# Optimization experiments

Measured on AMD Instinct MI355X. Metric: run time of the kernel, lower is better.

Reference implementation:

```python
import jax, jax.numpy as jnp
import numpy as np

N, EG, T, H, EC, L, NT = 10000, 200000, 300000, 128, 128, 3, 100


def _ssp(x):
    # ShiftedSoftplus: softplus(x) - log(2)
    return jax.nn.softplus(x) - jnp.log(2.0).astype(x.dtype)


def _bn(x, g, b):
    # BatchNorm1d in training mode: biased batch stats, eps=1e-5
    m = jnp.mean(x, axis=0)
    v = jnp.var(x, axis=0)
    return g * (x - m) * jax.lax.rsqrt(v + 1e-5) + b


def _forward(z, i, j, idx_i, idx_j, idx_k, idx_ji, idx_kj, pos,
             We1, be1, We2, be2, We3, be3,
             Wc1, bc1, g_c1, b_c1, g_n, b_n,
             Wc2, bc2, g_c2, b_c2, Wc3, bc3, g_c3, b_c3,
             g_c22, b_c22, g_c32, b_c32,
             Wf1, bf1, Wf2, bf2, Wf3, bf3):
    # AtomType2NodeEmb
    h = jax.nn.one_hot(z, NT, dtype=jnp.float32)
    h = _ssp(h @ We1 + be1)
    h = _ssp(h @ We2 + be2)
    node = h @ We3 + be3                      # [N, H]
    # geometry + GaussianFilter edge embedding
    rel = pos[i] - pos[j]                     # [EG, 3]
    dist = jnp.sqrt(jnp.sum(rel * rel, axis=-1))
    unit = rel / dist[:, None]
    offset = jnp.linspace(0.0, 5.0, EC)
    coeff = -0.5 / (offset[1] - offset[0]) ** 2
    edge = jnp.exp(coeff * (dist[:, None] - offset[None, :]) ** 2)  # [EG, EC]
    for l in range(L):
        # NodeUpdate
        c1 = jnp.concatenate([node[i], edge], axis=1) @ Wc1[l] + bc1[l]
        c1 = _bn(c1, g_c1[l], b_c1[l])
        f1, r1 = jnp.split(c1, 2, axis=1)
        agg = jax.ops.segment_sum(jax.nn.sigmoid(f1) * jnp.tanh(r1), i, num_segments=N)
        node = jnp.tanh(node + _bn(agg, g_n[l], b_n[l]))
        # EdgeUpdate: pair term
        c2 = (node[i] * node[j]) @ Wc2[l] + bc2[l]
        c2 = _bn(c2, g_c2[l], b_c2[l])
        f2, r2 = jnp.split(c2, 2, axis=1)
        c2_emb = _bn(jax.nn.sigmoid(f2) * jnp.tanh(r2), g_c22[l], b_c22[l])
        # EdgeUpdate: triplet term
        c3 = jnp.concatenate([node[idx_i], node[idx_j], node[idx_k],
                              edge[idx_ji], edge[idx_kj]], axis=1) @ Wc3[l] + bc3[l]
        c3 = _bn(c3, g_c3[l], b_c3[l])
        f3, r3 = jnp.split(c3, 2, axis=1)
        agg3 = jax.ops.segment_sum(jax.nn.sigmoid(f3) * jnp.tanh(r3), idx_ji, num_segments=EG)
        c3_emb = _bn(agg3, g_c32[l], b_c32[l])
        edge = jnp.tanh(edge + c2_emb + c3_emb)
    # ForcePredictor
    f = _ssp(edge @ Wf1 + bf1)
    f = _ssp(f @ Wf2 + bf2)
    force = (f @ Wf3 + bf3) * unit            # [EG, 3]
    return jax.ops.segment_sum(force, i, num_segments=N)


def setup_inputs() -> dict:
    ks = iter(jax.random.split(jax.random.key(0), 32))

    def w(shape):
        return jax.random.normal(next(ks), shape, jnp.float32) * (shape[-2] ** -0.5)

    z = jax.random.randint(next(ks), (N,), 0, NT)
    pos = jax.random.uniform(next(ks), (N, 3), jnp.float32) * 5.0
    i = jax.random.randint(next(ks), (EG,), 0, N)
    j = (i + 1 + jax.random.randint(next(ks), (EG,), 0, N - 1)) % N  # no self-loops
    idx_i = jax.random.randint(next(ks), (T,), 0, N)
    idx_j = jax.random.randint(next(ks), (T,), 0, N)
    idx_k = jax.random.randint(next(ks), (T,), 0, N)
    idx_ji = jax.random.randint(next(ks), (T,), 0, EG)
    idx_kj = jax.random.randint(next(ks), (T,), 0, EG)
    return dict(
        z=z, pos=pos, i=i, j=j, idx_i=idx_i, idx_j=idx_j, idx_k=idx_k,
        idx_ji=idx_ji, idx_kj=idx_kj,
        We1=w((NT, H)), be1=jnp.zeros((H,)), We2=w((H, H)), be2=jnp.zeros((H,)),
        We3=w((H, H)), be3=jnp.zeros((H,)),
        Wc1=w((L, H + EC, 2 * H)), bc1=jnp.zeros((L, 2 * H)),
        g_c1=jnp.ones((L, 2 * H)), b_c1=jnp.zeros((L, 2 * H)),
        g_n=jnp.ones((L, H)), b_n=jnp.zeros((L, H)),
        Wc2=w((L, H, 2 * EC)), bc2=jnp.zeros((L, 2 * EC)),
        g_c2=jnp.ones((L, 2 * EC)), b_c2=jnp.zeros((L, 2 * EC)),
        Wc3=w((L, 3 * H + 2 * EC, 2 * EC)), bc3=jnp.zeros((L, 2 * EC)),
        g_c3=jnp.ones((L, 2 * EC)), b_c3=jnp.zeros((L, 2 * EC)),
        g_c22=jnp.ones((L, EC)), b_c22=jnp.zeros((L, EC)),
        g_c32=jnp.ones((L, EC)), b_c32=jnp.zeros((L, EC)),
        Wf1=w((EC, EC)), bf1=jnp.zeros((EC,)), Wf2=w((EC, EC)), bf2=jnp.zeros((EC,)),
        Wf3=w((EC, 1)), bf3=jnp.zeros((1,)),
    )


def reference(z, pos, i, j, idx_i, idx_j, idx_k, idx_ji, idx_kj,
              We1, be1, We2, be2, We3, be3,
              Wc1, bc1, g_c1, b_c1, g_n, b_n,
              Wc2, bc2, g_c2, b_c2, Wc3, bc3, g_c3, b_c3,
              g_c22, b_c22, g_c32, b_c32,
              Wf1, bf1, Wf2, bf2, Wf3, bf3):
    return _forward(z, i, j, idx_i, idx_j, idx_k, idx_ji, idx_kj, pos,
                    We1, be1, We2, be2, We3, be3,
                    Wc1, bc1, g_c1, b_c1, g_n, b_n,
                    Wc2, bc2, g_c2, b_c2, Wc3, bc3, g_c3, b_c3,
                    g_c22, b_c22, g_c32, b_c32,
                    Wf1, bf1, Wf2, bf2, Wf3, bf3)
```

## Files before the change

kernel.cpp:

```cpp
#include <hip/hip_runtime.h>

typedef unsigned short u16;
typedef unsigned int   u32;
typedef __attribute__((ext_vector_type(8))) short short8;
typedef __attribute__((ext_vector_type(4))) float f32x4;

#define NN  10000
#define EGN 200000
#define TTN 300000
#define LLN 3

__device__ __forceinline__ float b2f(u16 u){ union{u32 i; float f;} x; x.i=(u32)u<<16; return x.f; }
__device__ __forceinline__ u16 f2b(float f){ union{float f; u32 u;} x; x.f=f; u32 r=(x.u + 0x7fffu + ((x.u>>16)&1u))>>16; return (u16)r; }
__device__ __forceinline__ float sigf(float x){ return 1.f/(1.f+__expf(-x)); }
__device__ __forceinline__ float tanhf_(float x){ float e=__expf(2.f*x); return 1.f - 2.f/(e+1.f); }
__device__ __forceinline__ float sspf(float x){ return fmaxf(x,0.f) + log1pf(__expf(-fabsf(x))) - 0.6931471805599453f; }

__device__ __forceinline__ void async16(void* lds, const void* g){
  __builtin_amdgcn_global_load_lds((const __attribute__((address_space(1))) void*)g,
                                   (__attribute__((address_space(3))) void*)lds, 16, 0, 0);
}
__device__ __forceinline__ void split_store(float v, u16* ph, u16* pl, size_t o){
  u16 h = f2b(v); ph[o] = h; pl[o] = f2b(v - b2f(h));
}
__device__ __forceinline__ short8 ldfrag(const u16* P, int row, int kk, int lane){
  int kg = kk*4 + (lane>>4);
  int slot = kg ^ (row&7);
  return *(const short8*)(P + row*64 + slot*8);
}

struct Segs {
  const u16* sh[10];
  const u16* sl[10];
  const int* idx[10];
  int coff[10];
};

template<int NP, int ROWS>
__device__ __forceinline__ void stageA(u16* Ah, u16* Al,
    const u16* sh, const u16* sl, const int* idxp, int coff,
    int rb, int M, int tid){
#pragma unroll
  for (int rnd=0; rnd<ROWS/32; ++rnd){
    int u = rnd*256 + tid;
    int row = u>>3, s = u&7, sw = s ^ (row&7);
    int grow = rb + row; if (grow >= M) grow = M-1;
    int srow = idxp ? idxp[grow] : grow;
    size_t go = (size_t)srow*256 + coff + sw*16;
    async16(Ah + u*8, (const char*)sh + go);
    if (NP==2) async16(Al + u*8, (const char*)sl + go);
  }
}

template<int NP, int ROWS>
__device__ __forceinline__ void stageA_prod(u16* Ah, u16* Al,
    const u16* nh, const u16* nl, const int* pii, const int* pjj,
    int rb, int M, int ks, int tid){
#pragma unroll
  for (int rep=0; rep<ROWS/64; ++rep){
    int row = rep*64 + (tid>>2), q = tid&3;
    int e = rb + row; if (e >= M) e = M-1;
    int ia = pii[e], ja = pjj[e];
    const u16* phi = nh + (size_t)ia*128 + ks*64 + q*16;
    const u16* pli = nl + (size_t)ia*128 + ks*64 + q*16;
    const u16* phj = nh + (size_t)ja*128 + ks*64 + q*16;
    const u16* plj = nl + (size_t)ja*128 + ks*64 + q*16;
#pragma unroll
    for (int c=0;c<2;c++){
      short8 hi = *(const short8*)(phi + c*8);
      short8 li = *(const short8*)(pli + c*8);
      short8 hj = *(const short8*)(phj + c*8);
      short8 lj = *(const short8*)(plj + c*8);
      short8 vh, vl;
#pragma unroll
      for (int k=0;k<8;k++){
        float a = b2f((u16)hi[k]) + b2f((u16)li[k]);
        float b = b2f((u16)hj[k]) + b2f((u16)lj[k]);
        float v = a*b;
        u16 h = f2b(v);
        vh[k] = (short)h;
        vl[k] = (short)f2b(v - b2f(h));
      }
      int g = q*2 + c, slot = g ^ (row&7);
      *(short8*)(Ah + row*64 + slot*8) = vh;
      if (NP==2) *(short8*)(Al + row*64 + slot*8) = vl;
    }
  }
}

template<int NP, int BROWS>
__device__ __forceinline__ void stageB_id(u16* Bh, u16* Bl,
    const u16* Wh, const u16* Wl, int K2b, int ksoff, int tid){
#pragma unroll
  for (int rnd=0; rnd<BROWS/32; ++rnd){
    int u = rnd*256 + tid;
    int row = u>>3, s = u&7, sw = s ^ (row&7);
    size_t go = (size_t)row*K2b + ksoff + sw*16;
    async16(Bh + u*8, (const char*)Wh + go);
    if (NP==2) async16(Bl + u*8, (const char*)Wl + go);
  }
}

template<int NP>
__device__ __forceinline__ void stageB_pair(u16* Bh, u16* Bl,
    const u16* Wh, const u16* Wl, int P0, int K2b, int ksoff, int tid){
#pragma unroll
  for (int rnd=0; rnd<4; ++rnd){
    int u = rnd*256 + tid;
    int row = u>>3, s = u&7, sw = s ^ (row&7);
    int wr = (row < 64) ? (P0 + row) : (128 + P0 + (row-64));
    size_t go = (size_t)wr*K2b + ksoff + sw*16;
    async16(Bh + u*8, (const char*)Wh + go);
    if (NP==2) async16(Bl + u*8, (const char*)Wl + go);
  }
}

template<bool PROD>
__global__ __launch_bounds__(256) void gemm_stats(
  int M, int nseg, Segs segs,
  const u16* __restrict__ nh, const u16* __restrict__ nl,
  const int* __restrict__ pii, const int* __restrict__ pjj,
  const u16* __restrict__ Wh, int K2b, const float* __restrict__ bias,
  float* __restrict__ st)
{
  __shared__ u16 Ah[64*64];
  __shared__ u16 Bh[256*64];
  __shared__ float ls[256], lq[256];
  const int tid = threadIdx.x, lane = tid&63, wv = tid>>6;
  const int rb = blockIdx.x*64;
  ls[tid]=0.f; lq[tid]=0.f;

  f32x4 acc[16];
#pragma unroll
  for (int n=0;n<16;n++) acc[n] = (f32x4){0.f,0.f,0.f,0.f};

  for (int ks=0; ks<nseg; ++ks){
    if (PROD) stageA_prod<1,64>(Ah, nullptr, nh, nl, pii, pjj, rb, M, ks, tid);
    else      stageA<1,64>(Ah, nullptr, segs.sh[ks], nullptr, segs.idx[ks], segs.coff[ks], rb, M, tid);
    stageB_id<1,256>(Bh, nullptr, Wh, nullptr, K2b, ks*128, tid);
    __syncthreads();
    const int arow = wv*16 + (lane&15);
#pragma unroll
    for (int kk=0;kk<2;kk++){
      short8 a = ldfrag(Ah, arow, kk, lane);
#pragma unroll
      for (int n=0;n<16;n++){
        short8 b = ldfrag(Bh, n*16 + (lane&15), kk, lane);
        acc[n] = __builtin_amdgcn_mfma_f32_16x16x32_bf16(a, b, acc[n], 0,0,0);
      }
    }
    __syncthreads();
  }
#pragma unroll
  for (int n=0;n<16;n++){
    float bb = bias[n*16 + (lane&15)];
    float s=0.f, q=0.f;
#pragma unroll
    for (int r=0;r<4;r++){
      int grow = rb + wv*16 + (lane>>4)*4 + r;
      if (grow < M){ float v = acc[n][r] + bb; s += v; q += v*v; }
    }
    s += __shfl_xor(s,16); s += __shfl_xor(s,32);
    q += __shfl_xor(q,16); q += __shfl_xor(q,32);
    if (lane < 16){ atomicAdd(&ls[n*16+lane], s); atomicAdd(&lq[n*16+lane], q); }
  }
  __syncthreads();
  atomicAdd(&st[tid], ls[tid]); atomicAdd(&st[256+tid], lq[tid]);
}

template<int NP, bool PROD, int EPI>
__global__ __launch_bounds__(256) void gemm_pair(
  int M, int nseg, Segs segs,
  const u16* __restrict__ nh, const u16* __restrict__ nl,
  const int* __restrict__ pii, const int* __restrict__ pjj,
  const u16* __restrict__ Wh, const u16* __restrict__ Wl, int K2b,
  const float* __restrict__ bias,
  const float* __restrict__ st, const float* __restrict__ g, const float* __restrict__ b, float inv,
  const int* __restrict__ sidx, float* __restrict__ aggout,
  const float* __restrict__ st22, const float* __restrict__ g22, const float* __restrict__ b22,
  const float* __restrict__ st32, const float* __restrict__ g32, const float* __restrict__ b32, float inv2,
  const float* __restrict__ agg3, u16* __restrict__ eh, u16* __restrict__ el,
  float* __restrict__ st22out)
{
  __shared__ u16 Ah[128*64];
  __shared__ u16 Al[NP==2 ? 128*64 : 64];
  __shared__ u16 Bh[128*64];
  __shared__ u16 Bl[NP==2 ? 128*64 : 64];
  __shared__ float ls[64], lq[64];
  __shared__ float sAf[64], sCf[64], sAr[64], sCr[64];
  __shared__ float sA22[64], sC22[64], sA32[64], sC32[64];
  const int tid = threadIdx.x, lane = tid&63, wv = tid>>6;
  const int wm = wv>>1, wn = wv&1;
  const int rb = blockIdx.x*128, P0 = blockIdx.y*64;

  if (tid < 64){
    int p = P0 + tid;
    float m1 = st[p]*inv,     v1 = st[256+p]*inv - m1*m1;
    float a1 = g[p]*rsqrtf(v1+1e-5f);
    sAf[tid]=a1; sCf[tid]=b[p]-a1*m1;
    float m2 = st[128+p]*inv, v2 = st[384+p]*inv - m2*m2;
    float a2 = g[128+p]*rsqrtf(v2+1e-5f);
    sAr[tid]=a2; sCr[tid]=b[128+p]-a2*m2;
    if (EPI==1){
      float m3 = st22[p]*inv2, v3 = st22[128+p]*inv2 - m3*m3;
      float a3 = g22[p]*rsqrtf(v3+1e-5f);
      sA22[tid]=a3; sC22[tid]=b22[p]-a3*m3;
      float m4 = st32[p]*inv2, v4 = st32[128+p]*inv2 - m4*m4;
      float a4 = g32[p]*rsqrtf(v4+1e-5f);
      sA32[tid]=a4; sC32[tid]=b32[p]-a4*m4;
    }
    if (EPI==2){ ls[tid]=0.f; lq[tid]=0.f; }
  }

  f32x4 accf[4][2], accr[4][2];
#pragma unroll
  for (int m=0;m<4;m++)
#pragma unroll
    for (int n=0;n<2;n++){ accf[m][n]=(f32x4){0.f,0.f,0.f,0.f}; accr[m][n]=(f32x4){0.f,0.f,0.f,0.f}; }

  for (int ks=0; ks<nseg; ++ks){
    if (PROD) stageA_prod<NP,128>(Ah, Al, nh, nl, pii, pjj, rb, M, ks, tid);
    else      stageA<NP,128>(Ah, Al, segs.sh[ks], segs.sl[ks], segs.idx[ks], segs.coff[ks], rb, M, tid);
    stageB_pair<NP>(Bh, Bl, Wh, Wl, P0, K2b, ks*128, tid);
    __syncthreads();
#pragma unroll
    for (int kk=0;kk<2;kk++){
      short8 ah[4], al[4];
#pragma unroll
      for (int m=0;m<4;m++){
        int ar = wm*64 + m*16 + (lane&15);
        ah[m] = ldfrag(Ah, ar, kk, lane);
        if constexpr (NP==2) al[m] = ldfrag(Al, ar, kk, lane);
      }
#pragma unroll
      for (int n=0;n<2;n++){
        int brf = wn*32 + n*16 + (lane&15);
        short8 bfh = ldfrag(Bh, brf,    kk, lane);
        short8 brh = ldfrag(Bh, 64+brf, kk, lane);
        short8 bfl, brl;
        if constexpr (NP==2){ bfl = ldfrag(Bl, brf, kk, lane); brl = ldfrag(Bl, 64+brf, kk, lane); }
#pragma unroll
        for (int m=0;m<4;m++){
          accf[m][n] = __builtin_amdgcn_mfma_f32_16x16x32_bf16(ah[m], bfh, accf[m][n], 0,0,0);
          accr[m][n] = __builtin_amdgcn_mfma_f32_16x16x32_bf16(ah[m], brh, accr[m][n], 0,0,0);
          if constexpr (NP==2){
            accf[m][n] = __builtin_amdgcn_mfma_f32_16x16x32_bf16(ah[m], bfl, accf[m][n], 0,0,0);
            accf[m][n] = __builtin_amdgcn_mfma_f32_16x16x32_bf16(al[m], bfh, accf[m][n], 0,0,0);
            accr[m][n] = __builtin_amdgcn_mfma_f32_16x16x32_bf16(ah[m], brl, accr[m][n], 0,0,0);
            accr[m][n] = __builtin_amdgcn_mfma_f32_16x16x32_bf16(al[m], brh, accr[m][n], 0,0,0);
          }
        }
      }
    }
    __syncthreads();
  }

#pragma unroll
  for (int n=0;n<2;n++){
    const int pp = wn*32 + n*16 + (lane&15);
    const int p  = P0 + pp;
    const float bf_ = bias[p], br_ = bias[128+p];
    const float Af = sAf[pp], Cf = sCf[pp], Ar = sAr[pp], Cr = sCr[pp];
    float su=0.f, sq=0.f;
#pragma unroll
    for (int m=0;m<4;m++){
#pragma unroll
      for (int r=0;r<4;r++){
        int grow = rb + wm*64 + m*16 + (lane>>4)*4 + r;
        if (grow < M){
          float yf = accf[m][n][r] + bf_;
          float yr = accr[m][n][r] + br_;
          float u = sigf(Af*yf + Cf) * tanhf_(Ar*yr + Cr);
          if (EPI==0){
            atomicAdd(&aggout[(size_t)sidx[grow]*128 + p], u);
          } else if (EPI==1){
            size_t o = (size_t)grow*128 + p;
            float eo = b2f(eh[o]) + b2f(el[o]);
            float v = tanhf_(eo + sA22[pp]*u + sC22[pp] + sA32[pp]*agg3[o] + sC32[pp]);
            split_store(v, eh, el, o);
          } else {
            su += u; sq += u*u;
          }
        }
      }
    }
    if (EPI==2){
      su += __shfl_xor(su,16); su += __shfl_xor(su,32);
      sq += __shfl_xor(sq,16); sq += __shfl_xor(sq,32);
      if (lane < 16){ atomicAdd(&ls[wn*32+n*16+lane], su); atomicAdd(&lq[wn*32+n*16+lane], sq); }
    }
  }
  if (EPI==2){
    __syncthreads();
    if (tid < 64){ atomicAdd(&st22out[P0+tid], ls[tid]); atomicAdd(&st22out[128+P0+tid], lq[tid]); }
  }
}

__global__ __launch_bounds__(256) void gemm_force(
  int M, Segs segs,
  const u16* __restrict__ Wh, const u16* __restrict__ Wl, int K2b,
  const float* __restrict__ bias, u16* __restrict__ oh, u16* __restrict__ ol)
{
  __shared__ u16 Ah[64*64], Al[64*64];
  __shared__ u16 Bh[128*64], Bl[128*64];
  const int tid = threadIdx.x, lane = tid&63, wv = tid>>6;
  const int rb = blockIdx.x*64;

  f32x4 acc[8];
#pragma unroll
  for (int n=0;n<8;n++) acc[n] = (f32x4){0.f,0.f,0.f,0.f};

  for (int ks=0; ks<2; ++ks){
    stageA<2,64>(Ah, Al, segs.sh[ks], segs.sl[ks], segs.idx[ks], segs.coff[ks], rb, M, tid);
    stageB_id<2,128>(Bh, Bl, Wh, Wl, K2b, ks*128, tid);
    __syncthreads();
    const int arow = wv*16 + (lane&15);
#pragma unroll
    for (int kk=0;kk<2;kk++){
      short8 ah = ldfrag(Ah, arow, kk, lane);
      short8 al = ldfrag(Al, arow, kk, lane);
#pragma unroll
      for (int n=0;n<8;n++){
        int br = n*16 + (lane&15);
        short8 bh = ldfrag(Bh, br, kk, lane);
        short8 bl = ldfrag(Bl, br, kk, lane);
        acc[n] = __builtin_amdgcn_mfma_f32_16x16x32_bf16(ah, bh, acc[n], 0,0,0);
        acc[n] = __builtin_amdgcn_mfma_f32_16x16x32_bf16(ah, bl, acc[n], 0,0,0);
        acc[n] = __builtin_amdgcn_mfma_f32_16x16x32_bf16(al, bh, acc[n], 0,0,0);
      }
    }
    __syncthreads();
  }
#pragma unroll
  for (int n=0;n<8;n++){
    int col = n*16 + (lane&15);
    float bb = bias[col];
#pragma unroll
    for (int r=0;r<4;r++){
      int grow = rb + wv*16 + (lane>>4)*4 + r;
      if (grow < M){
        float v = sspf(acc[n][r] + bb);
        split_store(v, oh, ol, (size_t)grow*128 + col);
      }
    }
  }
}

__global__ void transpose_cvt(const float* __restrict__ src, u16* __restrict__ dh, u16* __restrict__ dl, int K, int N){
  __shared__ float t[32][33];
  const float* s = src + (size_t)blockIdx.z * K * N;
  u16* dsth = dh + (size_t)blockIdx.z * K * N;
  u16* dstl = dl + (size_t)blockIdx.z * K * N;
  int n0 = blockIdx.x*32, k0 = blockIdx.y*32;
  for (int dy=threadIdx.y; dy<32; dy+=8){
    int k = k0+dy, n = n0+threadIdx.x;
    if (k<K && n<N) t[dy][threadIdx.x] = s[(size_t)k*N + n];
  }
  __syncthreads();
  for (int dy=threadIdx.y; dy<32; dy+=8){
    int n = n0+dy, k = k0+threadIdx.x;
    if (n<N && k<K) split_store(t[threadIdx.x][dy], dsth, dstl, (size_t)n*K + k);
  }
}

__global__ __launch_bounds__(128) void embed_k(const int* __restrict__ z,
  const float* __restrict__ We1, const float* __restrict__ be1,
  const float* __restrict__ We2, const float* __restrict__ be2,
  const float* __restrict__ We3, const float* __restrict__ be3,
  u16* __restrict__ nh, u16* __restrict__ nl){
  __shared__ float h0[128], h1[128];
  int nid = blockIdx.x, t = threadIdx.x;
  int zz = z[nid];
  h0[t] = sspf(We1[zz*128 + t] + be1[t]);
  __syncthreads();
  float a = be2[t];
  for (int k=0;k<128;k++) a += h0[k]*We2[k*128+t];
  h1[t] = sspf(a);
  __syncthreads();
  float b = be3[t];
  for (int k=0;k<128;k++) b += h1[k]*We3[k*128+t];
  split_store(b, nh, nl, (size_t)nid*128+t);
}

__global__ __launch_bounds__(256) void geom_k(const float* __restrict__ pos,
  const int* __restrict__ ii, const int* __restrict__ jj,
  float* __restrict__ unitv, u16* __restrict__ eh, u16* __restrict__ el){
  int t = threadIdx.x; int e = blockIdx.x*2 + (t>>7); int col = t&127;
  int a = ii[e], b = jj[e];
  float dx = pos[a*3]-pos[b*3], dy=pos[a*3+1]-pos[b*3+1], dz=pos[a*3+2]-pos[b*3+2];
  float dist = sqrtf(dx*dx+dy*dy+dz*dz);
  if (col==0){ float inv=1.f/dist; unitv[e*3]=dx*inv; unitv[e*3+1]=dy*inv; unitv[e*3+2]=dz*inv; }
  const float step = 5.0f/127.0f;
  const float coeff = -0.5f/(step*step);
  float d = dist - step*(float)col;
  float g = __expf(coeff*d*d);
  split_store(g, eh, el, (size_t)e*128+col);
}

__global__ __launch_bounds__(256) void colstats128(const float* __restrict__ m, int M, float* __restrict__ st){
  __shared__ float ls[128], lq[128];
  int t=threadIdx.x; if(t<128){ls[t]=0.f;lq[t]=0.f;} __syncthreads();
  int col=t&127, hf=t>>7; float ps=0.f,pq=0.f;
  int npair=(M+1)>>1;
  for (int pr=blockIdx.x; pr<npair; pr+=gridDim.x){
    int row=pr*2+hf;
    if(row<M){ float v=m[(size_t)row*128+col]; ps+=v; pq+=v*v; }
  }
  atomicAdd(&ls[col],ps); atomicAdd(&lq[col],pq);
  __syncthreads();
  if(t<128){ atomicAdd(&st[t],ls[t]); atomicAdd(&st[128+t],lq[t]); }
}

__global__ __launch_bounds__(256) void node_update_k(u16* __restrict__ nh, u16* __restrict__ nl,
  const float* __restrict__ agg, const float* __restrict__ st,
  const float* __restrict__ g, const float* __restrict__ b, float inv, int Nn)
{
  int t=threadIdx.x; int col=t&127, hf=t>>7;
  float mean = st[col]*inv;
  float var  = st[128+col]*inv - mean*mean;
  float A = g[col]*rsqrtf(var+1e-5f);
  float C = b[col] - A*mean;
  int npair=(Nn+1)>>1;
  for (int pr=blockIdx.x; pr<npair; pr+=gridDim.x){
    int row=pr*2+hf; if(row>=Nn) continue;
    size_t o=(size_t)row*128+col;
    float nv = b2f(nh[o]) + b2f(nl[o]);
    float v = tanhf_(nv + A*agg[o] + C);
    split_store(v, nh, nl, o);
  }
}

__global__ __launch_bounds__(256) void force_k(const u16* __restrict__ fh, const u16* __restrict__ fl,
  const float* __restrict__ Wf3, const float* __restrict__ bf3,
  const float* __restrict__ unitv, const int* __restrict__ ii, float* __restrict__ outp, int Me)
{
  int wv=threadIdx.x>>6, lane=threadIdx.x&63;
  int e = blockIdx.x*4 + wv; if(e>=Me) return;
  size_t o0=(size_t)e*128+lane, o1=o0+64;
  float p = (b2f(fh[o0])+b2f(fl[o0]))*Wf3[lane] + (b2f(fh[o1])+b2f(fl[o1]))*Wf3[64+lane];
  for (int s=32;s>0;s>>=1) p += __shfl_down(p, s);
  if (lane==0){
    float F = p + bf3[0];
    atomicAdd(&outp[ii[e]*3+0], F*unitv[e*3+0]);
    atomicAdd(&outp[ii[e]*3+1], F*unitv[e*3+1]);
    atomicAdd(&outp[ii[e]*3+2], F*unitv[e*3+2]);
  }
}

__global__ void sentinel_k(float* o, int n, float v){
  int i = blockIdx.x*256 + threadIdx.x; if (i<n) o[i]=v;
}

extern "C" void kernel_launch(void* const* d_in, const int* in_sizes, int n_in,
                              void* d_out, int out_size, void* d_ws, size_t ws_size,
                              hipStream_t stream)
{
  (void)in_sizes; (void)n_in;
  const int* z      = (const int*)d_in[0];
  const float* pos  = (const float*)d_in[1];
  const int* ii     = (const int*)d_in[2];
  const int* jj     = (const int*)d_in[3];
  const int* idx_i  = (const int*)d_in[4];
  const int* idx_j  = (const int*)d_in[5];
  const int* idx_k  = (const int*)d_in[6];
  const int* idx_ji = (const int*)d_in[7];
  const int* idx_kj = (const int*)d_in[8];
  const float* We1=(const float*)d_in[9];  const float* be1=(const float*)d_in[10];
  const float* We2=(const float*)d_in[11]; const float* be2=(const float*)d_in[12];
  const float* We3=(const float*)d_in[13]; const float* be3=(const float*)d_in[14];
  const float* Wc1=(const float*)d_in[15]; const float* bc1=(const float*)d_in[16];
  const float* g_c1=(const float*)d_in[17]; const float* b_c1=(const float*)d_in[18];
  const float* g_n=(const float*)d_in[19]; const float* b_n=(const float*)d_in[20];
  const float* Wc2=(const float*)d_in[21]; const float* bc2=(const float*)d_in[22];
  const float* g_c2=(const float*)d_in[23]; const float* b_c2=(const float*)d_in[24];
  const float* Wc3=(const float*)d_in[25]; const float* bc3=(const float*)d_in[26];
  const float* g_c3=(const float*)d_in[27]; const float* b_c3=(const float*)d_in[28];
  const float* g_c22=(const float*)d_in[29]; const float* b_c22=(const float*)d_in[30];
  const float* g_c32=(const float*)d_in[31]; const float* b_c32=(const float*)d_in[32];
  const float* Wf1=(const float*)d_in[33]; const float* bf1=(const float*)d_in[34];
  const float* Wf2=(const float*)d_in[35]; const float* bf2=(const float*)d_in[36];
  const float* Wf3=(const float*)d_in[37]; const float* bf3=(const float*)d_in[38];

  char* ws = (char*)d_ws;
  size_t off=0;
  auto alloc=[&](size_t b){ size_t o=off; off += (b+255)&~(size_t)255; return o; };
  u16*   node_h = (u16*)(ws + alloc((size_t)NN*128*2));
  u16*   node_l = (u16*)(ws + alloc((size_t)NN*128*2));
  u16*   edge_h = (u16*)(ws + alloc((size_t)EGN*128*2));
  u16*   edge_l = (u16*)(ws + alloc((size_t)EGN*128*2));
  float* unitv  = (float*)(ws + alloc((size_t)EGN*3*4));
  float* agg    = (float*)(ws + alloc((size_t)NN*128*4));
  float* agg3   = (float*)(ws + alloc((size_t)EGN*128*4));
  u16*   wc1h   = (u16*)(ws + alloc((size_t)3*256*256*2));
  u16*   wc1l   = (u16*)(ws + alloc((size_t)3*256*256*2));
  u16*   wc2h   = (u16*)(ws + alloc((size_t)3*256*128*2));
  u16*   wc2l   = (u16*)(ws + alloc((size_t)3*256*128*2));
  u16*   wc3h   = (u16*)(ws + alloc((size_t)3*256*640*2));
  u16*   wc3l   = (u16*)(ws + alloc((size_t)3*256*640*2));
  u16*   wf1h   = (u16*)(ws + alloc((size_t)128*128*2));
  u16*   wf1l   = (u16*)(ws + alloc((size_t)128*128*2));
  u16*   wf2h   = (u16*)(ws + alloc((size_t)128*128*2));
  u16*   wf2l   = (u16*)(ws + alloc((size_t)128*128*2));
  float* stats  = (float*)(ws + alloc(2304*4));

  if (off > ws_size){
    sentinel_k<<<(out_size+255)/256, 256, 0, stream>>>((float*)d_out, out_size, 123456.0f);
    return;
  }

  float* st1 = stats;
  float* st2 = stats+512;
  float* st3 = stats+1024;
  float* stN = stats+1536;
  float* st32= stats+1792;
  float* st22= stats+2048;

  u16* f1h = (u16*)agg3;
  u16* f1l = f1h + (size_t)EGN*128;
  u16* f2h = edge_h;
  u16* f2l = edge_l;

  hipMemsetAsync(d_out, 0, (size_t)out_size*4, stream);

  dim3 tb(32,8);
  transpose_cvt<<<dim3(8,8,3),  tb, 0, stream>>>(Wc1, wc1h, wc1l, 256, 256);
  transpose_cvt<<<dim3(8,4,3),  tb, 0, stream>>>(Wc2, wc2h, wc2l, 128, 256);
  transpose_cvt<<<dim3(8,20,3), tb, 0, stream>>>(Wc3, wc3h, wc3l, 640, 256);
  transpose_cvt<<<dim3(4,4,1),  tb, 0, stream>>>(Wf1, wf1h, wf1l, 128, 128);
  transpose_cvt<<<dim3(4,4,1),  tb, 0, stream>>>(Wf2, wf2h, wf2l, 128, 128);

  embed_k<<<NN,128,0,stream>>>(z, We1,be1,We2,be2,We3,be3, node_h, node_l);
  geom_k<<<EGN/2,256,0,stream>>>(pos, ii, jj, unitv, edge_h, edge_l);

  const int gE64  = (EGN+63)/64;
  const int gT64  = (TTN+63)/64;
  const int gE128 = (EGN+127)/128;
  const int gT128 = (TTN+127)/128;
  Segs dummy{};
  const float invE = 1.0f/EGN, invT = 1.0f/TTN, invN = 1.0f/NN;

  for (int l=0;l<LLN;l++){
    hipMemsetAsync(stats, 0, 2304*4, stream);
    hipMemsetAsync(agg,  0, (size_t)NN*128*4, stream);
    hipMemsetAsync(agg3, 0, (size_t)EGN*128*4, stream);

    const u16* w1h = wc1h + l*256*256; const u16* w1l = wc1l + l*256*256;
    const u16* w2h = wc2h + l*256*128; const u16* w2l = wc2l + l*256*128;
    const u16* w3h = wc3h + l*256*640; const u16* w3l = wc3l + l*256*640;

    Segs s1{};
    s1.sh[0]=node_h; s1.sl[0]=node_l; s1.idx[0]=ii;      s1.coff[0]=0;
    s1.sh[1]=node_h; s1.sl[1]=node_l; s1.idx[1]=ii;      s1.coff[1]=128;
    s1.sh[2]=edge_h; s1.sl[2]=edge_l; s1.idx[2]=nullptr; s1.coff[2]=0;
    s1.sh[3]=edge_h; s1.sl[3]=edge_l; s1.idx[3]=nullptr; s1.coff[3]=128;
    gemm_stats<false><<<gE64,256,0,stream>>>(EGN, 4, s1, nullptr,nullptr,nullptr,nullptr,
                                             w1h, 512, bc1+l*256, st1);
    gemm_pair<2,false,0><<<dim3(gE128,2),256,0,stream>>>(EGN, 4, s1, nullptr,nullptr,nullptr,nullptr,
        w1h, w1l, 512, bc1+l*256,
        st1, g_c1+l*256, b_c1+l*256, invE,
        ii, agg,
        nullptr,nullptr,nullptr, nullptr,nullptr,nullptr, 0.f,
        nullptr, nullptr, nullptr, nullptr);
    colstats128<<<256,256,0,stream>>>(agg, NN, stN);
    node_update_k<<<2048,256,0,stream>>>(node_h, node_l, agg, stN, g_n+l*128, b_n+l*128, invN, NN);

    Segs s3{};
    s3.sh[0]=node_h; s3.sl[0]=node_l; s3.idx[0]=idx_i;  s3.coff[0]=0;
    s3.sh[1]=node_h; s3.sl[1]=node_l; s3.idx[1]=idx_i;  s3.coff[1]=128;
    s3.sh[2]=node_h; s3.sl[2]=node_l; s3.idx[2]=idx_j;  s3.coff[2]=0;
    s3.sh[3]=node_h; s3.sl[3]=node_l; s3.idx[3]=idx_j;  s3.coff[3]=128;
    s3.sh[4]=node_h; s3.sl[4]=node_l; s3.idx[4]=idx_k;  s3.coff[4]=0;
    s3.sh[5]=node_h; s3.sl[5]=node_l; s3.idx[5]=idx_k;  s3.coff[5]=128;
    s3.sh[6]=edge_h; s3.sl[6]=edge_l; s3.idx[6]=idx_ji; s3.coff[6]=0;
    s3.sh[7]=edge_h; s3.sl[7]=edge_l; s3.idx[7]=idx_ji; s3.coff[7]=128;
    s3.sh[8]=edge_h; s3.sl[8]=edge_l; s3.idx[8]=idx_kj; s3.coff[8]=0;
    s3.sh[9]=edge_h; s3.sl[9]=edge_l; s3.idx[9]=idx_kj; s3.coff[9]=128;
    gemm_stats<false><<<gT64,256,0,stream>>>(TTN, 10, s3, nullptr,nullptr,nullptr,nullptr,
                                             w3h, 1280, bc3+l*256, st3);
    gemm_pair<2,false,0><<<dim3(gT128,2),256,0,stream>>>(TTN, 10, s3, nullptr,nullptr,nullptr,nullptr,
        w3h, w3l, 1280, bc3+l*256,
        st3, g_c3+l*256, b_c3+l*256, invT,
        idx_ji, agg3,
        nullptr,nullptr,nullptr, nullptr,nullptr,nullptr, 0.f,
        nullptr, nullptr, nullptr, nullptr);
    colstats128<<<1024,256,0,stream>>>(agg3, EGN, st32);

    gemm_stats<true><<<gE64,256,0,stream>>>(EGN, 2, dummy, node_h,node_l,ii,jj,
                                            w2h, 256, bc2+l*256, st2);
    gemm_pair<1,true,2><<<dim3(gE128,2),256,0,stream>>>(EGN, 2, dummy, node_h,node_l,ii,jj,
        w2h, nullptr, 256, bc2+l*256,
        st2, g_c2+l*256, b_c2+l*256, invE,
        nullptr, nullptr,
        nullptr,nullptr,nullptr, nullptr,nullptr,nullptr, 0.f,
        nullptr, nullptr, nullptr, st22);
    gemm_pair<2,true,1><<<dim3(gE128,2),256,0,stream>>>(EGN, 2, dummy, node_h,node_l,ii,jj,
        w2h, w2l, 256, bc2+l*256,
        st2, g_c2+l*256, b_c2+l*256, invE,
        nullptr, nullptr,
        st22, g_c22+l*128, b_c22+l*128, st32, g_c32+l*128, b_c32+l*128, invE,
        agg3, edge_h, edge_l, nullptr);
  }

  Segs sf1{}; sf1.sh[0]=edge_h; sf1.sl[0]=edge_l; sf1.idx[0]=nullptr; sf1.coff[0]=0;
              sf1.sh[1]=edge_h; sf1.sl[1]=edge_l; sf1.idx[1]=nullptr; sf1.coff[1]=128;
  gemm_force<<<gE64,256,0,stream>>>(EGN, sf1, wf1h, wf1l, 256, bf1, f1h, f1l);
  Segs sf2{}; sf2.sh[0]=f1h; sf2.sl[0]=f1l; sf2.idx[0]=nullptr; sf2.coff[0]=0;
              sf2.sh[1]=f1h; sf2.sl[1]=f1l; sf2.idx[1]=nullptr; sf2.coff[1]=128;
  gemm_force<<<gE64,256,0,stream>>>(EGN, sf2, wf2h, wf2l, 256, bf2, f2h, f2l);
  force_k<<<(EGN+3)/4,256,0,stream>>>(f2h, f2l, Wf3, bf3, unitv, ii, (float*)d_out, EGN);
}
```

Measured before the change: 4.618 ms.

## Remap wave tiling in GEMMs to share A fragments and shrink pair row tile

```diff
diff --git a/kernel.cpp b/kernel.cpp
--- a/kernel.cpp
+++ b/kernel.cpp
@@ -127,42 +127,52 @@
   __shared__ u16 Bh[256*64];
   __shared__ float ls[256], lq[256];
   const int tid = threadIdx.x, lane = tid&63, wv = tid>>6;
+  const int lane15 = lane&15;
   const int rb = blockIdx.x*64;
   ls[tid]=0.f; lq[tid]=0.f;
 
-  f32x4 acc[16];
-#pragma unroll
-  for (int n=0;n<16;n++) acc[n] = (f32x4){0.f,0.f,0.f,0.f};
+  f32x4 acc[4][4];
+#pragma unroll
+  for (int m=0;m<4;m++)
+#pragma unroll
+    for (int n=0;n<4;n++) acc[m][n] = (f32x4){0.f,0.f,0.f,0.f};
 
   for (int ks=0; ks<nseg; ++ks){
     if (PROD) stageA_prod<1,64>(Ah, nullptr, nh, nl, pii, pjj, rb, M, ks, tid);
     else      stageA<1,64>(Ah, nullptr, segs.sh[ks], nullptr, segs.idx[ks], segs.coff[ks], rb, M, tid);
     stageB_id<1,256>(Bh, nullptr, Wh, nullptr, K2b, ks*128, tid);
     __syncthreads();
-    const int arow = wv*16 + (lane&15);
 #pragma unroll
     for (int kk=0;kk<2;kk++){
-      short8 a = ldfrag(Ah, arow, kk, lane);
-#pragma unroll
-      for (int n=0;n<16;n++){
-        short8 b = ldfrag(Bh, n*16 + (lane&15), kk, lane);
-        acc[n] = __builtin_amdgcn_mfma_f32_16x16x32_bf16(a, b, acc[n], 0,0,0);
+      short8 a[4];
+#pragma unroll
+      for (int m=0;m<4;m++) a[m] = ldfrag(Ah, m*16 + lane15, kk, lane);
+#pragma unroll
+      for (int n=0;n<4;n++){
+        short8 b = ldfrag(Bh, wv*64 + n*16 + lane15, kk, lane);
+#pragma unroll
+        for (int m=0;m<4;m++)
+          acc[m][n] = __builtin_amdgcn_mfma_f32_16x16x32_bf16(a[m], b, acc[m][n], 0,0,0);
       }
     }
     __syncthreads();
   }
 #pragma unroll
-  for (int n=0;n<16;n++){
-    float bb = bias[n*16 + (lane&15)];
+  for (int n=0;n<4;n++){
+    int col = wv*64 + n*16 + lane15;
+    float bb = bias[col];
     float s=0.f, q=0.f;
 #pragma unroll
-    for (int r=0;r<4;r++){
-      int grow = rb + wv*16 + (lane>>4)*4 + r;
-      if (grow < M){ float v = acc[n][r] + bb; s += v; q += v*v; }
+    for (int m=0;m<4;m++){
+#pragma unroll
+      for (int r=0;r<4;r++){
+        int grow = rb + m*16 + (lane>>4)*4 + r;
+        if (grow < M){ float v = acc[m][n][r] + bb; s += v; q += v*v; }
+      }
     }
     s += __shfl_xor(s,16); s += __shfl_xor(s,32);
     q += __shfl_xor(q,16); q += __shfl_xor(q,32);
-    if (lane < 16){ atomicAdd(&ls[n*16+lane], s); atomicAdd(&lq[n*16+lane], q); }
+    if (lane < 16){ atomicAdd(&ls[wv*64 + n*16 + lane], s); atomicAdd(&lq[wv*64 + n*16 + lane], q); }
   }
   __syncthreads();
   atomicAdd(&st[tid], ls[tid]); atomicAdd(&st[256+tid], lq[tid]);
@@ -182,16 +192,16 @@
   const float* __restrict__ agg3, u16* __restrict__ eh, u16* __restrict__ el,
   float* __restrict__ st22out)
 {
-  __shared__ u16 Ah[128*64];
-  __shared__ u16 Al[NP==2 ? 128*64 : 64];
+  __shared__ u16 Ah[64*64];
+  __shared__ u16 Al[NP==2 ? 64*64 : 64];
   __shared__ u16 Bh[128*64];
   __shared__ u16 Bl[NP==2 ? 128*64 : 64];
   __shared__ float ls[64], lq[64];
   __shared__ float sAf[64], sCf[64], sAr[64], sCr[64];
   __shared__ float sA22[64], sC22[64], sA32[64], sC32[64];
   const int tid = threadIdx.x, lane = tid&63, wv = tid>>6;
-  const int wm = wv>>1, wn = wv&1;
-  const int rb = blockIdx.x*128, P0 = blockIdx.y*64;
+  const int lane15 = lane&15;
+  const int rb = blockIdx.x*64, P0 = blockIdx.y*64;
 
   if (tid < 64){
     int p = P0 + tid;
@@ -212,15 +222,13 @@
     if (EPI==2){ ls[tid]=0.f; lq[tid]=0.f; }
   }
 
-  f32x4 accf[4][2], accr[4][2];
-#pragma unroll
-  for (int m=0;m<4;m++)
-#pragma unroll
-    for (int n=0;n<2;n++){ accf[m][n]=(f32x4){0.f,0.f,0.f,0.f}; accr[m][n]=(f32x4){0.f,0.f,0.f,0.f}; }
+  f32x4 accf[4], accr[4];
+#pragma unroll
+  for (int m=0;m<4;m++){ accf[m]=(f32x4){0.f,0.f,0.f,0.f}; accr[m]=(f32x4){0.f,0.f,0.f,0.f}; }
 
   for (int ks=0; ks<nseg; ++ks){
-    if (PROD) stageA_prod<NP,128>(Ah, Al, nh, nl, pii, pjj, rb, M, ks, tid);
-    else      stageA<NP,128>(Ah, Al, segs.sh[ks], segs.sl[ks], segs.idx[ks], segs.coff[ks], rb, M, tid);
+    if (PROD) stageA_prod<NP,64>(Ah, Al, nh, nl, pii, pjj, rb, M, ks, tid);
+    else      stageA<NP,64>(Ah, Al, segs.sh[ks], segs.sl[ks], segs.idx[ks], segs.coff[ks], rb, M, tid);
     stageB_pair<NP>(Bh, Bl, Wh, Wl, P0, K2b, ks*128, tid);
     __syncthreads();
 #pragma unroll
@@ -228,69 +236,61 @@
       short8 ah[4], al[4];
 #pragma unroll
       for (int m=0;m<4;m++){
-        int ar = wm*64 + m*16 + (lane&15);
-        ah[m] = ldfrag(Ah, ar, kk, lane);
-        if constexpr (NP==2) al[m] = ldfrag(Al, ar, kk, lane);
-      }
-#pragma unroll
-      for (int n=0;n<2;n++){
-        int brf = wn*32 + n*16 + (lane&15);
-        short8 bfh = ldfrag(Bh, brf,    kk, lane);
-        short8 brh = ldfrag(Bh, 64+brf, kk, lane);
-        short8 bfl, brl;
-        if constexpr (NP==2){ bfl = ldfrag(Bl, brf, kk, lane); brl = ldfrag(Bl, 64+brf, kk, lane); }
-#pragma unroll
-        for (int m=0;m<4;m++){
-          accf[m][n] = __builtin_amdgcn_mfma_f32_16x16x32_bf16(ah[m], bfh, accf[m][n], 0,0,0);
-          accr[m][n] = __builtin_amdgcn_mfma_f32_16x16x32_bf16(ah[m], brh, accr[m][n], 0,0,0);
-          if constexpr (NP==2){
-            accf[m][n] = __builtin_amdgcn_mfma_f32_16x16x32_bf16(ah[m], bfl, accf[m][n], 0,0,0);
-            accf[m][n] = __builtin_amdgcn_mfma_f32_16x16x32_bf16(al[m], bfh, accf[m][n], 0,0,0);
-            accr[m][n] = __builtin_amdgcn_mfma_f32_16x16x32_bf16(ah[m], brl, accr[m][n], 0,0,0);
-            accr[m][n] = __builtin_amdgcn_mfma_f32_16x16x32_bf16(al[m], brh, accr[m][n], 0,0,0);
-          }
+        ah[m] = ldfrag(Ah, m*16 + lane15, kk, lane);
+        if constexpr (NP==2) al[m] = ldfrag(Al, m*16 + lane15, kk, lane);
+      }
+      short8 bfh = ldfrag(Bh, wv*16 + lane15,      kk, lane);
+      short8 brh = ldfrag(Bh, 64 + wv*16 + lane15, kk, lane);
+      short8 bfl, brl;
+      if constexpr (NP==2){
+        bfl = ldfrag(Bl, wv*16 + lane15,      kk, lane);
+        brl = ldfrag(Bl, 64 + wv*16 + lane15, kk, lane);
+      }
+#pragma unroll
+      for (int m=0;m<4;m++){
+        accf[m] = __builtin_amdgcn_mfma_f32_16x16x32_bf16(ah[m], bfh, accf[m], 0,0,0);
+        accr[m] = __builtin_amdgcn_mfma_f32_16x16x32_bf16(ah[m], brh, accr[m], 0,0,0);
+        if constexpr (NP==2){
+          accf[m] = __builtin_amdgcn_mfma_f32_16x16x32_bf16(ah[m], bfl, accf[m], 0,0,0);
+          accf[m] = __builtin_amdgcn_mfma_f32_16x16x32_bf16(al[m], bfh, accf[m], 0,0,0);
+          accr[m] = __builtin_amdgcn_mfma_f32_16x16x32_bf16(ah[m], brl, accr[m], 0,0,0);
+          accr[m] = __builtin_amdgcn_mfma_f32_16x16x32_bf16(al[m], brh, accr[m], 0,0,0);
         }
       }
     }
     __syncthreads();
   }
 
-#pragma unroll
-  for (int n=0;n<2;n++){
-    const int pp = wn*32 + n*16 + (lane&15);
-    const int p  = P0 + pp;
-    const float bf_ = bias[p], br_ = bias[128+p];
-    const float Af = sAf[pp], Cf = sCf[pp], Ar = sAr[pp], Cr = sCr[pp];
-    float su=0.f, sq=0.f;
-#pragma unroll
-    for (int m=0;m<4;m++){
-#pragma unroll
-      for (int r=0;r<4;r++){
-        int grow = rb + wm*64 + m*16 + (lane>>4)*4 + r;
-        if (grow < M){
-          float yf = accf[m][n][r] + bf_;
-          float yr = accr[m][n][r] + br_;
-          float u = sigf(Af*yf + Cf) * tanhf_(Ar*yr + Cr);
-          if (EPI==0){
-            atomicAdd(&aggout[(size_t)sidx[grow]*128 + p], u);
-          } else if (EPI==1){
-            size_t o = (size_t)grow*128 + p;
-            float eo = b2f(eh[o]) + b2f(el[o]);
-            float v = tanhf_(eo + sA22[pp]*u + sC22[pp] + sA32[pp]*agg3[o] + sC32[pp]);
-            split_store(v, eh, el, o);
-          } else {
-            su += u; sq += u*u;
-          }
-        }
-      }
-    }
-    if (EPI==2){
-      su += __shfl_xor(su,16); su += __shfl_xor(su,32);
-      sq += __shfl_xor(sq,16); sq += __shfl_xor(sq,32);
-      if (lane < 16){ atomicAdd(&ls[wn*32+n*16+lane], su); atomicAdd(&lq[wn*32+n*16+lane], sq); }
+  const int pp = wv*16 + lane15;
+  const int p  = P0 + pp;
+  const float bf_ = bias[p], br_ = bias[128+p];
+  const float Af = sAf[pp], Cf = sCf[pp], Ar = sAr[pp], Cr = sCr[pp];
+  float su=0.f, sq=0.f;
+#pragma unroll
+  for (int m=0;m<4;m++){
+#pragma unroll
+    for (int r=0;r<4;r++){
+      int grow = rb + m*16 + (lane>>4)*4 + r;
+      if (grow >= M) continue;
+      float yf = accf[m][r] + bf_;
+      float yr = accr[m][r] + br_;
+      float u = sigf(Af*yf + Cf) * tanhf_(Ar*yr + Cr);
+      if (EPI==0){
+        atomicAdd(&aggout[(size_t)sidx[grow]*128 + p], u);
+      } else if (EPI==1){
+        size_t o = (size_t)grow*128 + p;
+        float eo = b2f(eh[o]) + b2f(el[o]);
+        float v = tanhf_(eo + sA22[pp]*u + sC22[pp] + sA32[pp]*agg3[o] + sC32[pp]);
+        split_store(v, eh, el, o);
+      } else {
+        su += u; sq += u*u;
+      }
     }
   }
   if (EPI==2){
+    su += __shfl_xor(su,16); su += __shfl_xor(su,32);
+    sq += __shfl_xor(sq,16); sq += __shfl_xor(sq,32);
+    if (lane < 16){ atomicAdd(&ls[wv*16+lane], su); atomicAdd(&lq[wv*16+lane], sq); }
     __syncthreads();
     if (tid < 64){ atomicAdd(&st22out[P0+tid], ls[tid]); atomicAdd(&st22out[128+P0+tid], lq[tid]); }
   }
@@ -304,43 +304,54 @@
   __shared__ u16 Ah[64*64], Al[64*64];
   __shared__ u16 Bh[128*64], Bl[128*64];
   const int tid = threadIdx.x, lane = tid&63, wv = tid>>6;
+  const int lane15 = lane&15;
   const int rb = blockIdx.x*64;
 
-  f32x4 acc[8];
-#pragma unroll
-  for (int n=0;n<8;n++) acc[n] = (f32x4){0.f,0.f,0.f,0.f};
+  f32x4 acc[4][2];
+#pragma unroll
+  for (int m=0;m<4;m++)
+#pragma unroll
+    for (int n=0;n<2;n++) acc[m][n] = (f32x4){0.f,0.f,0.f,0.f};
 
   for (int ks=0; ks<2; ++ks){
     stageA<2,64>(Ah, Al, segs.sh[ks], segs.sl[ks], segs.idx[ks], segs.coff[ks], rb, M, tid);
     stageB_id<2,128>(Bh, Bl, Wh, Wl, K2b, ks*128, tid);
     __syncthreads();
-    const int arow = wv*16 + (lane&15);
 #pragma unroll
     for (int kk=0;kk<2;kk++){
-      short8 ah = ldfrag(Ah, arow, kk, lane);
-      short8 al = ldfrag(Al, arow, kk, lane);
-#pragma unroll
-      for (int n=0;n<8;n++){
-        int br = n*16 + (lane&15);
-        short8 bh = ldfrag(Bh, br, kk, lane);
-        short8 bl = ldfrag(Bl, br, kk, lane);
-        acc[n] = __builtin_amdgcn_mfma_f32_16x16x32_bf16(ah, bh, acc[n], 0,0,0);
-        acc[n] = __builtin_amdgcn_mfma_f32_16x16x32_bf16(ah, bl, acc[n], 0,0,0);
-        acc[n] = __builtin_amdgcn_mfma_f32_16x16x32_bf16(al, bh, acc[n], 0,0,0);
+      short8 ah[4], al[4];
+#pragma unroll
+      for (int m=0;m<4;m++){
+        ah[m] = ldfrag(Ah, m*16 + lane15, kk, lane);
+        al[m] = ldfrag(Al, m*16 + lane15, kk, lane);
+      }
+#pragma unroll
+      for (int n=0;n<2;n++){
+        short8 bh = ldfrag(Bh, wv*32 + n*16 + lane15, kk, lane);
+        short8 bl = ldfrag(Bl, wv*32 + n*16 + lane15, kk, lane);
+#pragma unroll
+        for (int m=0;m<4;m++){
+          acc[m][n] = __builtin_amdgcn_mfma_f32_16x16x32_bf16(ah[m], bh, acc[m][n], 0,0,0);
+          acc[m][n] = __builtin_amdgcn_mfma_f32_16x16x32_bf16(ah[m], bl, acc[m][n], 0,0,0);
+          acc[m][n] = __builtin_amdgcn_mfma_f32_16x16x32_bf16(al[m], bh, acc[m][n], 0,0,0);
+        }
       }
     }
     __syncthreads();
   }
 #pragma unroll
-  for (int n=0;n<8;n++){
-    int col = n*16 + (lane&15);
+  for (int n=0;n<2;n++){
+    int col = wv*32 + n*16 + lane15;
     float bb = bias[col];
 #pragma unroll
-    for (int r=0;r<4;r++){
-      int grow = rb + wv*16 + (lane>>4)*4 + r;
-      if (grow < M){
-        float v = sspf(acc[n][r] + bb);
-        split_store(v, oh, ol, (size_t)grow*128 + col);
+    for (int m=0;m<4;m++){
+#pragma unroll
+      for (int r=0;r<4;r++){
+        int grow = rb + m*16 + (lane>>4)*4 + r;
+        if (grow < M){
+          float v = sspf(acc[m][n][r] + bb);
+          split_store(v, oh, ol, (size_t)grow*128 + col);
+        }
       }
     }
   }
@@ -483,7 +494,7 @@
 
   char* ws = (char*)d_ws;
   size_t off=0;
-  auto alloc=[&](size_t b){ size_t o=off; off += (b+255)&~(size_t)255; return o; };
+  auto alloc=[&](size_t bb){ size_t o=off; off += (bb+255)&~(size_t)255; return o; };
   u16*   node_h = (u16*)(ws + alloc((size_t)NN*128*2));
   u16*   node_l = (u16*)(ws + alloc((size_t)NN*128*2));
   u16*   edge_h = (u16*)(ws + alloc((size_t)EGN*128*2));
@@ -534,8 +545,6 @@
 
   const int gE64  = (EGN+63)/64;
   const int gT64  = (TTN+63)/64;
-  const int gE128 = (EGN+127)/128;
-  const int gT128 = (TTN+127)/128;
   Segs dummy{};
   const float invE = 1.0f/EGN, invT = 1.0f/TTN, invN = 1.0f/NN;
 
@@ -555,7 +564,7 @@
     s1.sh[3]=edge_h; s1.sl[3]=edge_l; s1.idx[3]=nullptr; s1.coff[3]=128;
     gemm_stats<false><<<gE64,256,0,stream>>>(EGN, 4, s1, nullptr,nullptr,nullptr,nullptr,
                                              w1h, 512, bc1+l*256, st1);
-    gemm_pair<2,false,0><<<dim3(gE128,2),256,0,stream>>>(EGN, 4, s1, nullptr,nullptr,nullptr,nullptr,
+    gemm_pair<2,false,0><<<dim3(gE64,2),256,0,stream>>>(EGN, 4, s1, nullptr,nullptr,nullptr,nullptr,
         w1h, w1l, 512, bc1+l*256,
         st1, g_c1+l*256, b_c1+l*256, invE,
         ii, agg,
@@ -577,7 +586,7 @@
     s3.sh[9]=edge_h; s3.sl[9]=edge_l; s3.idx[9]=idx_kj; s3.coff[9]=128;
     gemm_stats<false><<<gT64,256,0,stream>>>(TTN, 10, s3, nullptr,nullptr,nullptr,nullptr,
                                              w3h, 1280, bc3+l*256, st3);
-    gemm_pair<2,false,0><<<dim3(gT128,2),256,0,stream>>>(TTN, 10, s3, nullptr,nullptr,nullptr,nullptr,
+    gemm_pair<2,false,0><<<dim3(gT64,2),256,0,stream>>>(TTN, 10, s3, nullptr,nullptr,nullptr,nullptr,
         w3h, w3l, 1280, bc3+l*256,
         st3, g_c3+l*256, b_c3+l*256, invT,
         idx_ji, agg3,
@@ -587,13 +596,13 @@
 
     gemm_stats<true><<<gE64,256,0,stream>>>(EGN, 2, dummy, node_h,node_l,ii,jj,
                                             w2h, 256, bc2+l*256, st2);
-    gemm_pair<1,true,2><<<dim3(gE128,2),256,0,stream>>>(EGN, 2, dummy, node_h,node_l,ii,jj,
+    gemm_pair<1,true,2><<<dim3(gE64,2),256,0,stream>>>(EGN, 2, dummy, node_h,node_l,ii,jj,
         w2h, nullptr, 256, bc2+l*256,
         st2, g_c2+l*256, b_c2+l*256, invE,
         nullptr, nullptr,
         nullptr,nullptr,nullptr, nullptr,nullptr,nullptr, 0.f,
         nullptr, nullptr, nullptr, st22);
-    gemm_pair<2,true,1><<<dim3(gE128,2),256,0,stream>>>(EGN, 2, dummy, node_h,node_l,ii,jj,
+    gemm_pair<2,true,1><<<dim3(gE64,2),256,0,stream>>>(EGN, 2, dummy, node_h,node_l,ii,jj,
         w2h, w2l, 256, bc2+l*256,
         st2, g_c2+l*256, b_c2+l*256, invE,
         nullptr, nullptr,
```

After: 4.164 ms (median of 2 runs). 9.8% less time.
